# Kernel tuning notes

Measured on AMD Instinct MI355X. Metric: run time of the kernel, lower is better.

The kernel has to match this reference:

```python
import jax, jax.numpy as jnp
import numpy as np

EPS = 1e-5  # haiku LayerNorm default eps

def _ln(x):
    # LayerNorm over last dim, no scale/offset, use_fast_variance=False
    m = jnp.mean(x, axis=-1, keepdims=True)
    v = jnp.mean((x - m) ** 2, axis=-1, keepdims=True)
    return (x - m) / jnp.sqrt(v + EPS)

def _adaptive_ln(x, cond, gamma_c, Ws, bs, Wb):
    # AdaptiveLayerNorm with single_cond path
    xn = _ln(x)
    cn = _ln(cond) * gamma_c           # single_cond_layer_norm (scale only)
    scale = cn @ Ws + bs               # single_cond_scale (with bias)
    bias = cn @ Wb                     # single_cond_bias (no bias)
    return jax.nn.sigmoid(scale) * xn + bias

def setup_inputs() -> dict:
    key = jax.random.key(0)
    ks = jax.random.split(key, 24)
    B, Q, K, C, H = 2, 3072, 3072, 128, 4
    Dh = C // H
    s = 0.02
    inp = {
        'x_q': jax.random.normal(ks[0], (B, Q, C), jnp.float32),
        'x_k': jax.random.normal(ks[1], (B, K, C), jnp.float32),
        'mask_q': jax.random.randint(ks[2], (B, Q), 0, 2, jnp.int32),
        'mask_k': jax.random.randint(ks[3], (B, K), 0, 2, jnp.int32),
        'pair_logits': jax.random.normal(ks[4], (B, H, Q, K), jnp.float32),
        'single_cond_q': jax.random.normal(ks[5], (B, Q, C), jnp.float32),
        'single_cond_k': jax.random.normal(ks[6], (B, K, C), jnp.float32),
        # AdaptiveLayerNorm q params
        'gamma_cq': jnp.ones((C,), jnp.float32),
        'Wsq': jax.random.normal(ks[7], (C, C), jnp.float32) * s,
        'bsq': jax.random.normal(ks[8], (C,), jnp.float32) * s,
        'Wbq': jax.random.normal(ks[9], (C, C), jnp.float32) * s,
        # AdaptiveLayerNorm k params
        'gamma_ck': jnp.ones((C,), jnp.float32),
        'Wsk': jax.random.normal(ks[10], (C, C), jnp.float32) * s,
        'bsk': jax.random.normal(ks[11], (C,), jnp.float32) * s,
        'Wbk': jax.random.normal(ks[12], (C, C), jnp.float32) * s,
        # attention projections
        'Wq': jax.random.normal(ks[13], (C, H, Dh), jnp.float32) * s,
        'bq': jax.random.normal(ks[14], (1, H, Dh), jnp.float32) * s,
        'Wk': jax.random.normal(ks[15], (C, H, Dh), jnp.float32) * s,
        'Wv': jax.random.normal(ks[16], (C, H, Dh), jnp.float32) * s,
        'Wg': jax.random.normal(ks[17], (C, C), jnp.float32) * s,
        # AdaptiveZeroInit params
        'Wt2': jax.random.normal(ks[18], (C, C), jnp.float32) * s,
        'Wzc': jax.random.normal(ks[19], (C, C), jnp.float32) * s,
        'bzc': jax.random.normal(ks[20], (C,), jnp.float32) * s,
    }
    return inp

def reference(x_q, x_k, mask_q, mask_k, pair_logits, single_cond_q, single_cond_k,
              gamma_cq, Wsq, bsq, Wbq, gamma_ck, Wsk, bsk, Wbk,
              Wq, bq, Wk, Wv, Wg, Wt2, Wzc, bzc):
    mq = mask_q.astype(jnp.float32)
    mk = mask_k.astype(jnp.float32)
    # bias as written in the original: 1e9 * (mq-1)[...,None,:,None] * (mk-1)[...,None,None,:]
    bias = 1e9 * (mq - 1.0)[:, None, :, None] * (mk - 1.0)[:, None, None, :]
    bias = bias + pair_logits  # [B,H,Q,K]

    xq = _adaptive_ln(x_q, single_cond_q, gamma_cq, Wsq, bsq, Wbq)
    xk = _adaptive_ln(x_k, single_cond_k, gamma_ck, Wsk, bsk, Wbk)

    Dh = Wq.shape[-1]
    q = jnp.einsum('bqi,ihd->bqhd', xq, Wq) + bq  # bq [1,H,Dh] broadcasts
    k = jnp.einsum('bki,ihd->bkhd', xk, Wk)
    v = jnp.einsum('bki,ihd->bkhd', xk, Wv)

    logits = jnp.einsum('bqhd,bkhd->bhqk', q * (Dh ** -0.5), k) + bias
    weights = jax.nn.softmax(logits, axis=-1).astype(xq.dtype)
    wa = jnp.einsum('bhqk,bkhd->bqhd', weights, v)
    B, Q, H, _ = wa.shape
    wa = wa.reshape(B, Q, H * Dh)

    wa = wa * jax.nn.sigmoid(xq @ Wg)  # gating_query

    # AdaptiveZeroInit with raw single_cond_q
    out = (wa @ Wt2) * jax.nn.sigmoid(single_cond_q @ Wzc + bzc)
    return out
```

## Files before the change

kernel.cpp:

```cpp
#include <hip/hip_runtime.h>
#include <hip/hip_bf16.h>

typedef unsigned short u16;
typedef unsigned int u32;
typedef __attribute__((ext_vector_type(4))) float f32x4;
typedef __attribute__((ext_vector_type(4))) u32 u32x4;
typedef __attribute__((ext_vector_type(2))) u32 u32x2;
typedef __attribute__((ext_vector_type(8))) __bf16 bf16x8;

#define SQ 3072
#define NH 4
#define DH 32

static __device__ __forceinline__ u16 f2bf(float f) {
  return __builtin_bit_cast(u16, (__bf16)f);
}
static __device__ __forceinline__ u32 pk2(float a, float b) {
  return (u32)f2bf(a) | ((u32)f2bf(b) << 16);
}
static __device__ __forceinline__ bf16x8 ld8(const u16* p) {
  return __builtin_bit_cast(bf16x8, *reinterpret_cast<const u32x4*>(p));
}
static __device__ __forceinline__ f32x4 mfma16(bf16x8 a, bf16x8 b, f32x4 c) {
  return __builtin_amdgcn_mfma_f32_16x16x32_bf16(a, b, c, 0, 0, 0);
}
static __device__ __forceinline__ float sigm(float x) { return 1.0f / (1.0f + __expf(-x)); }
static __device__ __forceinline__ float red16(float v) {
  v += __shfl_xor(v, 1); v += __shfl_xor(v, 2);
  v += __shfl_xor(v, 4); v += __shfl_xor(v, 8);
  return v;
}

static __device__ __forceinline__ void gemm8(
    const u16* a, const u16* wt, int lr, int lg, int w, f32x4 d[2]) {
  f32x4 z = {0.f, 0.f, 0.f, 0.f};
  d[0] = z; d[1] = z;
#pragma unroll
  for (int kc = 0; kc < 4; ++kc) {
    int ko = kc * 32 + lg * 8;
    bf16x8 a0 = ld8(a + lr * 136 + ko);
    bf16x8 a1 = ld8(a + (16 + lr) * 136 + ko);
    bf16x8 b0 = ld8(wt + (w * 16 + lr) * 128 + ko);
    d[0] = mfma16(a0, b0, d[0]);
    d[1] = mfma16(a1, b0, d[1]);
  }
}

struct PrepSrc { const float* p[10]; };

__global__ __launch_bounds__(256) void prep(PrepSrc s, u16* __restrict__ dst) {
  __shared__ float tl[32][132];
  const int mm = blockIdx.x >> 2, c = blockIdx.x & 3;
  const int tid = threadIdx.x;
  {
    const int krl = tid >> 3, col0 = (tid & 7) * 16;
    const int kr = c * 32 + krl;
    const float* src = s.p[mm] + kr * 128 + col0;
#pragma unroll
    for (int j = 0; j < 4; ++j) {
      f32x4 v = *reinterpret_cast<const f32x4*>(src + j * 4);
      tl[krl][col0 + j * 4 + 0] = v[0];
      tl[krl][col0 + j * 4 + 1] = v[1];
      tl[krl][col0 + j * 4 + 2] = v[2];
      tl[krl][col0 + j * 4 + 3] = v[3];
    }
  }
  __syncthreads();
  const int co = tid >> 1, kc0 = (tid & 1) * 16;
  u32 wbuf[8];
#pragma unroll
  for (int j = 0; j < 8; ++j)
    wbuf[j] = pk2(tl[kc0 + 2 * j][co], tl[kc0 + 2 * j + 1][co]);
  u32x4* dp = reinterpret_cast<u32x4*>(dst + mm * 16384 + co * 128 + c * 32 + kc0);
  u32x4 w0 = {wbuf[0], wbuf[1], wbuf[2], wbuf[3]};
  u32x4 w1 = {wbuf[4], wbuf[5], wbuf[6], wbuf[7]};
  dp[0] = w0; dp[1] = w1;
}

__global__ __launch_bounds__(512) void rowblocks(
    const float* __restrict__ x_q, const float* __restrict__ scq,
    const float* __restrict__ gamma_cq, const float* __restrict__ bsq,
    const float* __restrict__ bq, const float* __restrict__ bzc,
    const float* __restrict__ x_k, const float* __restrict__ sck,
    const float* __restrict__ gamma_ck, const float* __restrict__ bsk,
    const u16* __restrict__ WT, const int* __restrict__ mask_k,
    u16* __restrict__ qbf, float* __restrict__ gate, float* __restrict__ zc,
    u16* __restrict__ kbf, u16* __restrict__ vT, float* __restrict__ mkf) {
  __shared__ float xnf[32 * 132];
  __shared__ u16 a_cn[32 * 136];
  __shared__ u16 a_raw[32 * 136];
  __shared__ u16 a_xa[32 * 136];
  const int tid = threadIdx.x;
  const bool qside = blockIdx.x < 192;
  const int blk = qside ? blockIdx.x : blockIdx.x - 192;
  const float* x     = qside ? x_q : x_k;
  const float* cond  = qside ? scq : sck;
  const float* gamma = qside ? gamma_cq : gamma_ck;
  const float* bs    = qside ? bsq : bsk;
  const int rl = tid >> 4, sub = tid & 15, c0 = sub * 8;
  const size_t grow = (size_t)blk * 32 + rl;
  if (!qside && tid < 32) {
    size_t g2 = (size_t)blk * 32 + tid;
    mkf[g2] = (float)mask_k[g2] - 1.f;
  }

  {
    float xs[8];
    const float4* xr = reinterpret_cast<const float4*>(x + grow * 128 + c0);
    float4 t0 = xr[0], t1 = xr[1];
    xs[0]=t0.x; xs[1]=t0.y; xs[2]=t0.z; xs[3]=t0.w;
    xs[4]=t1.x; xs[5]=t1.y; xs[6]=t1.z; xs[7]=t1.w;
    float s = 0.f;
#pragma unroll
    for (int i = 0; i < 8; ++i) s += xs[i];
    float mean = red16(s) * (1.f / 128.f);
    float vs = 0.f;
#pragma unroll
    for (int i = 0; i < 8; ++i) { float dd = xs[i] - mean; vs += dd * dd; }
    float rstd = rsqrtf(red16(vs) * (1.f / 128.f) + 1e-5f);
    float4* xw = reinterpret_cast<float4*>(&xnf[rl * 132 + c0]);
    float4 o0, o1;
    o0.x=(xs[0]-mean)*rstd; o0.y=(xs[1]-mean)*rstd; o0.z=(xs[2]-mean)*rstd; o0.w=(xs[3]-mean)*rstd;
    o1.x=(xs[4]-mean)*rstd; o1.y=(xs[5]-mean)*rstd; o1.z=(xs[6]-mean)*rstd; o1.w=(xs[7]-mean)*rstd;
    xw[0] = o0; xw[1] = o1;
  }
  {
    float cs[8], gs[8];
    const float4* cr = reinterpret_cast<const float4*>(cond + grow * 128 + c0);
    const float4* gr = reinterpret_cast<const float4*>(gamma + c0);
    float4 c_0 = cr[0], c_1 = cr[1], g_0 = gr[0], g_1 = gr[1];
    cs[0]=c_0.x; cs[1]=c_0.y; cs[2]=c_0.z; cs[3]=c_0.w;
    cs[4]=c_1.x; cs[5]=c_1.y; cs[6]=c_1.z; cs[7]=c_1.w;
    gs[0]=g_0.x; gs[1]=g_0.y; gs[2]=g_0.z; gs[3]=g_0.w;
    gs[4]=g_1.x; gs[5]=g_1.y; gs[6]=g_1.z; gs[7]=g_1.w;
    float s = 0.f;
#pragma unroll
    for (int i = 0; i < 8; ++i) s += cs[i];
    float mean = red16(s) * (1.f / 128.f);
    float vs = 0.f;
#pragma unroll
    for (int i = 0; i < 8; ++i) { float dd = cs[i] - mean; vs += dd * dd; }
    float rstd = rsqrtf(red16(vs) * (1.f / 128.f) + 1e-5f);
    float cn[8];
#pragma unroll
    for (int i = 0; i < 8; ++i) cn[i] = (cs[i] - mean) * rstd * gs[i];
    u32x4 cw = {pk2(cn[0],cn[1]), pk2(cn[2],cn[3]), pk2(cn[4],cn[5]), pk2(cn[6],cn[7])};
    *reinterpret_cast<u32x4*>(&a_cn[rl * 136 + c0]) = cw;
    if (qside) {
      u32x4 rw = {pk2(cs[0],cs[1]), pk2(cs[2],cs[3]), pk2(cs[4],cs[5]), pk2(cs[6],cs[7])};
      *reinterpret_cast<u32x4*>(&a_raw[rl * 136 + c0]) = rw;
    }
  }
  __syncthreads();
  const int lane = tid & 63, w = tid >> 6, lr = lane & 15, lg = lane >> 4;
  const int wtbase = qside ? 0 : 5;
  f32x4 dS[2], dB[2];
  gemm8(a_cn, WT + (wtbase + 0) * 16384, lr, lg, w, dS);
  gemm8(a_cn, WT + (wtbase + 1) * 16384, lr, lg, w, dB);
  const int col = w * 16 + lr;
#pragma unroll
  for (int mt = 0; mt < 2; ++mt)
#pragma unroll
    for (int r = 0; r < 4; ++r) {
      int rowl = mt * 16 + lg * 4 + r;
      float sc = dS[mt][r] + bs[col];
      float xa = sigm(sc) * xnf[rowl * 132 + col] + dB[mt][r];
      a_xa[rowl * 136 + col] = f2bf(xa);
    }
  __syncthreads();
  if (qside) {
    f32x4 dQ[2], dG[2], dZ[2];
    gemm8(a_xa,  WT + 2 * 16384, lr, lg, w, dQ);
    gemm8(a_xa,  WT + 3 * 16384, lr, lg, w, dG);
    gemm8(a_raw, WT + 4 * 16384, lr, lg, w, dZ);
#pragma unroll
    for (int mt = 0; mt < 2; ++mt)
#pragma unroll
      for (int r = 0; r < 4; ++r) {
        int rowl = mt * 16 + lg * 4 + r;
        size_t gr = (size_t)blk * 32 + rowl;
        int b = (int)(gr >= SQ);
        int pos = (int)gr - b * SQ;
        float qv = (dQ[mt][r] + bq[col]) * 0.17677669529663687f;
        qbf[(((size_t)b * NH + (col >> 5)) * SQ + pos) * DH + (col & 31)] = f2bf(qv);
        gate[gr * 128 + col] = sigm(dG[mt][r]);
        zc[gr * 128 + col] = sigm(dZ[mt][r] + bzc[col]);
      }
  } else {
    f32x4 dK[2], dV[2];
    gemm8(a_xa, WT + 7 * 16384, lr, lg, w, dK);
    gemm8(a_xa, WT + 8 * 16384, lr, lg, w, dV);
    const int h = col >> 5, dd = col & 31;
#pragma unroll
    for (int mt = 0; mt < 2; ++mt)
#pragma unroll
      for (int r = 0; r < 4; ++r) {
        int rowl = mt * 16 + lg * 4 + r;
        size_t gr = (size_t)blk * 32 + rowl;
        int b = (int)(gr >= SQ);
        int pos = (int)gr - b * SQ;
        kbf[(((size_t)b * NH + h) * SQ + pos) * DH + dd] = f2bf(dK[mt][r]);
        vT[(((size_t)b * NH + h) * DH + dd) * SQ + pos] = f2bf(dV[mt][r]);
      }
  }
}

__global__ __launch_bounds__(256) void attn(
    const u16* __restrict__ qbf, const u16* __restrict__ kbf, const u16* __restrict__ vT,
    const float* __restrict__ pair, const int* __restrict__ mask_q,
    const float* __restrict__ mkf, const float* __restrict__ gate,
    u16* __restrict__ wa) {
  __shared__ u16 pbuf[2][16][264];
  __shared__ __align__(16) char un[4][2304];
  const int tid = threadIdx.x, lane = tid & 63, w = tid >> 6, lr = lane & 15, lg = lane >> 4;
  const int bid = blockIdx.x;
  const int bh = bid & 7, qt = bid >> 3;
  const int b = bh >> 2, h = bh & 3;
  const int q0 = qt * 16;
  const bf16x8 aq = ld8(qbf + ((size_t)bh * SQ + q0 + lr) * DH + lg * 8);
  const float mqm1 = 1e9f * ((float)mask_q[b * SQ + q0 + lr] - 1.f);
  float m = -1e30f, lsum = 0.f;
  const f32x4 zero = {0.f, 0.f, 0.f, 0.f};
  f32x4 o[2]; o[0] = zero; o[1] = zero;
  const float* prow0 = pair + ((size_t)bh * SQ + q0 + w * 4) * SQ;
  const float* mrow = mkf + b * SQ;
  u16* pw = reinterpret_cast<u16*>(un[w]);
  f32x4 pf[4];
#pragma unroll
  for (int j = 0; j < 4; ++j)
    pf[j] = __builtin_nontemporal_load(
        reinterpret_cast<const f32x4*>(prow0 + (size_t)j * SQ + lane * 4));
  for (int t = 0; t < 12; ++t) {
    const int bsel = t & 1;
#pragma unroll
    for (int j = 0; j < 4; ++j) {
      u32x2 pb = {pk2(pf[j][0], pf[j][1]), pk2(pf[j][2], pf[j][3])};
      *reinterpret_cast<u32x2*>(&pbuf[bsel][w * 4 + j][lane * 4]) = pb;
    }
    __syncthreads();
    if (t < 11) {
#pragma unroll
      for (int j = 0; j < 4; ++j)
        pf[j] = __builtin_nontemporal_load(
            reinterpret_cast<const f32x4*>(prow0 + (size_t)j * SQ + (t + 1) * 256 + lane * 4));
    }
    const int kb = t * 256 + w * 64;
    f32x4 s[4];
#pragma unroll
    for (int kt = 0; kt < 4; ++kt) {
      bf16x8 kfv = ld8(kbf + ((size_t)bh * SQ + kb + kt * 16 + lr) * DH + lg * 8);
      u32x2 pd = *reinterpret_cast<const u32x2*>(&pbuf[bsel][lr][w * 64 + kt * 16 + lg * 4]);
      f32x4 pv;
      pv[0] = __builtin_bit_cast(float, (pd[0] & 0xFFFFu) << 16);
      pv[1] = __builtin_bit_cast(float, pd[0] & 0xFFFF0000u);
      pv[2] = __builtin_bit_cast(float, (pd[1] & 0xFFFFu) << 16);
      pv[3] = __builtin_bit_cast(float, pd[1] & 0xFFFF0000u);
      f32x4 mk = *reinterpret_cast<const f32x4*>(mrow + kb + kt * 16 + lg * 4);
      f32x4 c;
      c[0] = fmaf(mqm1, mk[0], pv[0]); c[1] = fmaf(mqm1, mk[1], pv[1]);
      c[2] = fmaf(mqm1, mk[2], pv[2]); c[3] = fmaf(mqm1, mk[3], pv[3]);
      s[kt] = mfma16(kfv, aq, c);
    }
    f32x4 mx = s[0];
#pragma unroll
    for (int kt = 1; kt < 4; ++kt)
#pragma unroll
      for (int r = 0; r < 4; ++r) mx[r] = fmaxf(mx[r], s[kt][r]);
    float pm = fmaxf(fmaxf(mx[0], mx[1]), fmaxf(mx[2], mx[3]));
    pm = fmaxf(pm, __shfl_xor(pm, 16));
    pm = fmaxf(pm, __shfl_xor(pm, 32));
    if (!__all(pm <= m + 8.f)) {
      const float mn = fmaxf(m, pm);
      const float alpha = __expf(m - mn);
      m = mn;
      float al[4];
#pragma unroll
      for (int r = 0; r < 4; ++r)
        al[r] = __builtin_bit_cast(
            float, __builtin_amdgcn_ds_bpermute((lg * 4 + r) << 2,
                                                __builtin_bit_cast(int, alpha)));
#pragma unroll
      for (int hf = 0; hf < 2; ++hf)
#pragma unroll
        for (int r = 0; r < 4; ++r) o[hf][r] *= al[r];
      lsum *= alpha;
    }
    float ps = 0.f;
#pragma unroll
    for (int kt = 0; kt < 4; ++kt)
#pragma unroll
      for (int r = 0; r < 4; ++r) {
        float p = __expf(s[kt][r] - m);
        s[kt][r] = p;
        ps += p;
      }
    lsum += ps;
#pragma unroll
    for (int kt = 0; kt < 4; ++kt) {
      u32x2 pk = {pk2(s[kt][0], s[kt][1]), pk2(s[kt][2], s[kt][3])};
      *reinterpret_cast<u32x2*>(pw + lr * 72 + kt * 16 + lg * 4) = pk;
    }
#pragma unroll
    for (int kc = 0; kc < 2; ++kc) {
      bf16x8 pa = ld8(pw + lr * 72 + kc * 32 + lg * 8);
#pragma unroll
      for (int hf = 0; hf < 2; ++hf) {
        bf16x8 bv = ld8(vT + ((size_t)bh * DH + hf * 16 + lr) * SQ + kb + kc * 32 + lg * 8);
        o[hf] = mfma16(pa, bv, o[hf]);
      }
    }
  }
  lsum += __shfl_xor(lsum, 16);
  lsum += __shfl_xor(lsum, 32);
  float* mbw = reinterpret_cast<float*>(un[w]);
#pragma unroll
  for (int r = 0; r < 4; ++r) {
    int row = lg * 4 + r;
    mbw[row * 34 + lr] = o[0][r];
    mbw[row * 34 + 16 + lr] = o[1][r];
  }
  if (lane < 16) { mbw[lane * 34 + 32] = m; mbw[lane * 34 + 33] = lsum; }
  __syncthreads();
#pragma unroll
  for (int it = 0; it < 2; ++it) {
    int q = (tid >> 5) + it * 8;
    int d = tid & 31;
    float mm = -1e30f;
#pragma unroll
    for (int w4 = 0; w4 < 4; ++w4)
      mm = fmaxf(mm, reinterpret_cast<const float*>(un[w4])[q * 34 + 32]);
    float ll = 0.f, oo = 0.f;
#pragma unroll
    for (int w4 = 0; w4 < 4; ++w4) {
      const float* mb4 = reinterpret_cast<const float*>(un[w4]);
      float e = __expf(mb4[q * 34 + 32] - mm);
      ll = fmaf(e, mb4[q * 34 + 33], ll);
      oo = fmaf(e, mb4[q * 34 + d], oo);
    }
    size_t gi = ((size_t)b * SQ + q0 + q) * 128 + h * 32 + d;
    wa[gi] = f2bf((oo / ll) * gate[gi]);
  }
}

__global__ __launch_bounds__(512) void finalk(
    const u16* __restrict__ wa, const u16* __restrict__ WTt2,
    const float* __restrict__ zc, float* __restrict__ out) {
  __shared__ u16 awa[32 * 136];
  const int tid = threadIdx.x, rl = tid >> 4, sub = tid & 15, c0 = sub * 8;
  const size_t grow = (size_t)blockIdx.x * 32 + rl;
  *reinterpret_cast<u32x4*>(&awa[rl * 136 + c0]) =
      *reinterpret_cast<const u32x4*>(wa + grow * 128 + c0);
  __syncthreads();
  const int lane = tid & 63, w = tid >> 6, lr = lane & 15, lg = lane >> 4;
  f32x4 d[2];
  gemm8(awa, WTt2, lr, lg, w, d);
  const int col = w * 16 + lr;
#pragma unroll
  for (int mt = 0; mt < 2; ++mt)
#pragma unroll
    for (int r = 0; r < 4; ++r) {
      size_t gr = (size_t)blockIdx.x * 32 + mt * 16 + lg * 4 + r;
      out[gr * 128 + col] = d[mt][r] * zc[gr * 128 + col];
    }
}

extern "C" void kernel_launch(void* const* d_in, const int* in_sizes, int n_in,
                              void* d_out, int out_size, void* d_ws, size_t ws_size,
                              hipStream_t stream) {
  const float* x_q   = (const float*)d_in[0];
  const float* x_k   = (const float*)d_in[1];
  const int* mask_q  = (const int*)d_in[2];
  const int* mask_k  = (const int*)d_in[3];
  const float* pair  = (const float*)d_in[4];
  const float* scq   = (const float*)d_in[5];
  const float* sck   = (const float*)d_in[6];
  const float* gamma_cq = (const float*)d_in[7];
  const float* Wsq   = (const float*)d_in[8];
  const float* bsq   = (const float*)d_in[9];
  const float* Wbq   = (const float*)d_in[10];
  const float* gamma_ck = (const float*)d_in[11];
  const float* Wsk   = (const float*)d_in[12];
  const float* bsk   = (const float*)d_in[13];
  const float* Wbk   = (const float*)d_in[14];
  const float* Wq    = (const float*)d_in[15];
  const float* bq    = (const float*)d_in[16];
  const float* Wk    = (const float*)d_in[17];
  const float* Wv    = (const float*)d_in[18];
  const float* Wg    = (const float*)d_in[19];
  const float* Wt2   = (const float*)d_in[20];
  const float* Wzc   = (const float*)d_in[21];
  const float* bzc   = (const float*)d_in[22];

  char* wsb = (char*)d_ws;
  u16* WT     = (u16*)(wsb);
  u16* qbf    = (u16*)(wsb + 327680);
  u16* kbf    = (u16*)(wsb + 1900544);
  u16* vT     = (u16*)(wsb + 3473408);
  float* gate = (float*)(wsb + 5046272);
  float* zc   = (float*)(wsb + 8192000);
  u16* wa     = (u16*)(wsb + 11337728);
  float* mkf  = (float*)(wsb + 12910592);
  float* out  = (float*)d_out;

  PrepSrc ps;
  ps.p[0] = Wsq; ps.p[1] = Wbq; ps.p[2] = Wq; ps.p[3] = Wg; ps.p[4] = Wzc;
  ps.p[5] = Wsk; ps.p[6] = Wbk; ps.p[7] = Wk; ps.p[8] = Wv; ps.p[9] = Wt2;

  hipLaunchKernelGGL(prep, dim3(40), dim3(256), 0, stream, ps, WT);
  hipLaunchKernelGGL(rowblocks, dim3(384), dim3(512), 0, stream,
                     x_q, scq, gamma_cq, bsq, bq, bzc,
                     x_k, sck, gamma_ck, bsk, WT, mask_k,
                     qbf, gate, zc, kbf, vT, mkf);
  hipLaunchKernelGGL(attn, dim3(8 * 192), dim3(256), 0, stream,
                     qbf, kbf, vT, pair, mask_q, mkf, gate, wa);
  hipLaunchKernelGGL(finalk, dim3(192), dim3(512), 0, stream, wa, WT + 9 * 16384, zc, out);
}
```

Before: 117.4 us.

## Deepen pair-logit prefetch pipeline to triple-buffered LDS with two register sets

The attention kernel's streaming of pair logits moves from a double-buffered LDS with one register prefetch stage to a triple-buffered LDS fed by two alternating register sets. Global loads are issued up to four tiles ahead, and the loop is fully unrolled. The aim is to hide HBM latency on the dominant pair_logits read, which is about 300MB of fp32. The cost is more VGPRs and more LDS per block, which may lower occupancy.

```diff
diff --git a/kernel.cpp b/kernel.cpp
--- a/kernel.cpp
+++ b/kernel.cpp
@@ -210,7 +210,7 @@
     const float* __restrict__ pair, const int* __restrict__ mask_q,
     const float* __restrict__ mkf, const float* __restrict__ gate,
     u16* __restrict__ wa) {
-  __shared__ u16 pbuf[2][16][264];
+  __shared__ u16 pbuf[3][16][264];
   __shared__ __align__(16) char un[4][2304];
   const int tid = threadIdx.x, lane = tid & 63, w = tid >> 6, lr = lane & 15, lg = lane >> 4;
   const int bid = blockIdx.x;
@@ -225,31 +225,37 @@
   const float* prow0 = pair + ((size_t)bh * SQ + q0 + w * 4) * SQ;
   const float* mrow = mkf + b * SQ;
   u16* pw = reinterpret_cast<u16*>(un[w]);
-  f32x4 pf[4];
-#pragma unroll
-  for (int j = 0; j < 4; ++j)
-    pf[j] = __builtin_nontemporal_load(
-        reinterpret_cast<const f32x4*>(prow0 + (size_t)j * SQ + lane * 4));
+
+  f32x4 pA[4], pB[4];
+#define ISSUE(g, R)                                                              \
+  {                                                                              \
+    _Pragma("unroll") for (int j = 0; j < 4; ++j) R[j] =                         \
+        __builtin_nontemporal_load(reinterpret_cast<const f32x4*>(               \
+            prow0 + (size_t)j * SQ + (g) * 256 + lane * 4));                     \
+  }
+#define STORE(g, R)                                                              \
+  {                                                                              \
+    _Pragma("unroll") for (int j = 0; j < 4; ++j) {                              \
+      u32x2 pb = {pk2(R[j][0], R[j][1]), pk2(R[j][2], R[j][3])};                 \
+      *reinterpret_cast<u32x2*>(&pbuf[(g) % 3][w * 4 + j][lane * 4]) = pb;       \
+    }                                                                            \
+  }
+  ISSUE(0, pA); ISSUE(1, pB);
+  STORE(0, pA); ISSUE(2, pA);
+  STORE(1, pB); ISSUE(3, pB);
+#pragma unroll
   for (int t = 0; t < 12; ++t) {
-    const int bsel = t & 1;
-#pragma unroll
-    for (int j = 0; j < 4; ++j) {
-      u32x2 pb = {pk2(pf[j][0], pf[j][1]), pk2(pf[j][2], pf[j][3])};
-      *reinterpret_cast<u32x2*>(&pbuf[bsel][w * 4 + j][lane * 4]) = pb;
-    }
     __syncthreads();
-    if (t < 11) {
-#pragma unroll
-      for (int j = 0; j < 4; ++j)
-        pf[j] = __builtin_nontemporal_load(
-            reinterpret_cast<const f32x4*>(prow0 + (size_t)j * SQ + (t + 1) * 256 + lane * 4));
+    if (t + 2 < 12) {
+      if ((t & 1) == 0) { STORE(t + 2, pA); if (t + 4 < 12) ISSUE(t + 4, pA); }
+      else              { STORE(t + 2, pB); if (t + 4 < 12) ISSUE(t + 4, pB); }
     }
     const int kb = t * 256 + w * 64;
     f32x4 s[4];
 #pragma unroll
     for (int kt = 0; kt < 4; ++kt) {
       bf16x8 kfv = ld8(kbf + ((size_t)bh * SQ + kb + kt * 16 + lr) * DH + lg * 8);
-      u32x2 pd = *reinterpret_cast<const u32x2*>(&pbuf[bsel][lr][w * 64 + kt * 16 + lg * 4]);
+      u32x2 pd = *reinterpret_cast<const u32x2*>(&pbuf[t % 3][lr][w * 64 + kt * 16 + lg * 4]);
       f32x4 pv;
       pv[0] = __builtin_bit_cast(float, (pd[0] & 0xFFFFu) << 16);
       pv[1] = __builtin_bit_cast(float, pd[0] & 0xFFFF0000u);
@@ -310,6 +316,8 @@
       }
     }
   }
+#undef ISSUE
+#undef STORE
   lsum += __shfl_xor(lsum, 16);
   lsum += __shfl_xor(lsum, 32);
   float* mbw = reinterpret_cast<float*>(un[w]);
```

Result: no change. 118.9 us (+1.3%).

## Process 32 query rows per attention block to reuse K, V and mask loads

Applied to the files above, without the earlier changes.

Each attention workgroup now handles two 16-row query groups instead of one, so every K tile, V tile and key-mask vector loaded from global memory feeds two MFMA groups. The grid halves to 768 blocks, and each thread prefetches twice as many pair_logits rows. The pair_logits loads also switch from nontemporal to normal loads. The cost is higher register and LDS use per block, which may lower occupancy, and fewer blocks to spread across the CUs.

```diff
diff --git a/kernel.cpp b/kernel.cpp
--- a/kernel.cpp
+++ b/kernel.cpp
@@ -210,119 +210,154 @@
     const float* __restrict__ pair, const int* __restrict__ mask_q,
     const float* __restrict__ mkf, const float* __restrict__ gate,
     u16* __restrict__ wa) {
-  __shared__ u16 pbuf[2][16][264];
-  __shared__ __align__(16) char un[4][2304];
+  __shared__ u16 pbuf[2][32][264];
+  __shared__ __align__(16) char un[4][4608];
   const int tid = threadIdx.x, lane = tid & 63, w = tid >> 6, lr = lane & 15, lg = lane >> 4;
   const int bid = blockIdx.x;
   const int bh = bid & 7, qt = bid >> 3;
   const int b = bh >> 2, h = bh & 3;
-  const int q0 = qt * 16;
-  const bf16x8 aq = ld8(qbf + ((size_t)bh * SQ + q0 + lr) * DH + lg * 8);
-  const float mqm1 = 1e9f * ((float)mask_q[b * SQ + q0 + lr] - 1.f);
-  float m = -1e30f, lsum = 0.f;
+  const int q0 = qt * 32;
+  bf16x8 aq[2];
+  float mqm1[2];
+#pragma unroll
+  for (int qg = 0; qg < 2; ++qg) {
+    aq[qg] = ld8(qbf + ((size_t)bh * SQ + q0 + qg * 16 + lr) * DH + lg * 8);
+    mqm1[qg] = 1e9f * ((float)mask_q[b * SQ + q0 + qg * 16 + lr] - 1.f);
+  }
+  float m[2] = {-1e30f, -1e30f}, lsum[2] = {0.f, 0.f};
   const f32x4 zero = {0.f, 0.f, 0.f, 0.f};
-  f32x4 o[2]; o[0] = zero; o[1] = zero;
-  const float* prow0 = pair + ((size_t)bh * SQ + q0 + w * 4) * SQ;
+  f32x4 o[2][2];
+  o[0][0] = zero; o[0][1] = zero; o[1][0] = zero; o[1][1] = zero;
+  const float* prow0 = pair + ((size_t)bh * SQ + q0 + w * 8) * SQ;
   const float* mrow = mkf + b * SQ;
   u16* pw = reinterpret_cast<u16*>(un[w]);
-  f32x4 pf[4];
-#pragma unroll
-  for (int j = 0; j < 4; ++j)
-    pf[j] = __builtin_nontemporal_load(
-        reinterpret_cast<const f32x4*>(prow0 + (size_t)j * SQ + lane * 4));
+  f32x4 pf[8];
+#pragma unroll
+  for (int j = 0; j < 8; ++j)
+    pf[j] = *reinterpret_cast<const f32x4*>(prow0 + (size_t)j * SQ + lane * 4);
   for (int t = 0; t < 12; ++t) {
     const int bsel = t & 1;
 #pragma unroll
-    for (int j = 0; j < 4; ++j) {
+    for (int j = 0; j < 8; ++j) {
       u32x2 pb = {pk2(pf[j][0], pf[j][1]), pk2(pf[j][2], pf[j][3])};
-      *reinterpret_cast<u32x2*>(&pbuf[bsel][w * 4 + j][lane * 4]) = pb;
+      *reinterpret_cast<u32x2*>(&pbuf[bsel][w * 8 + j][lane * 4]) = pb;
     }
     __syncthreads();
     if (t < 11) {
 #pragma unroll
-      for (int j = 0; j < 4; ++j)
-        pf[j] = __builtin_nontemporal_load(
-            reinterpret_cast<const f32x4*>(prow0 + (size_t)j * SQ + (t + 1) * 256 + lane * 4));
+      for (int j = 0; j < 8; ++j)
+        pf[j] = *reinterpret_cast<const f32x4*>(prow0 + (size_t)j * SQ + (t + 1) * 256 + lane * 4);
     }
     const int kb = t * 256 + w * 64;
-    f32x4 s[4];
+    bf16x8 kf[4];
+    f32x4 mk[4];
 #pragma unroll
     for (int kt = 0; kt < 4; ++kt) {
-      bf16x8 kfv = ld8(kbf + ((size_t)bh * SQ + kb + kt * 16 + lr) * DH + lg * 8);
-      u32x2 pd = *reinterpret_cast<const u32x2*>(&pbuf[bsel][lr][w * 64 + kt * 16 + lg * 4]);
-      f32x4 pv;
-      pv[0] = __builtin_bit_cast(float, (pd[0] & 0xFFFFu) << 16);
-      pv[1] = __builtin_bit_cast(float, pd[0] & 0xFFFF0000u);
-      pv[2] = __builtin_bit_cast(float, (pd[1] & 0xFFFFu) << 16);
-      pv[3] = __builtin_bit_cast(float, pd[1] & 0xFFFF0000u);
-      f32x4 mk = *reinterpret_cast<const f32x4*>(mrow + kb + kt * 16 + lg * 4);
-      f32x4 c;
-      c[0] = fmaf(mqm1, mk[0], pv[0]); c[1] = fmaf(mqm1, mk[1], pv[1]);
-      c[2] = fmaf(mqm1, mk[2], pv[2]); c[3] = fmaf(mqm1, mk[3], pv[3]);
-      s[kt] = mfma16(kfv, aq, c);
-    }
-    f32x4 mx = s[0];
-#pragma unroll
-    for (int kt = 1; kt < 4; ++kt)
-#pragma unroll
-      for (int r = 0; r < 4; ++r) mx[r] = fmaxf(mx[r], s[kt][r]);
-    float pm = fmaxf(fmaxf(mx[0], mx[1]), fmaxf(mx[2], mx[3]));
-    pm = fmaxf(pm, __shfl_xor(pm, 16));
-    pm = fmaxf(pm, __shfl_xor(pm, 32));
-    if (!__all(pm <= m + 8.f)) {
-      const float mn = fmaxf(m, pm);
-      const float alpha = __expf(m - mn);
-      m = mn;
-      float al[4];
-#pragma unroll
-      for (int r = 0; r < 4; ++r)
-        al[r] = __builtin_bit_cast(
-            float, __builtin_amdgcn_ds_bpermute((lg * 4 + r) << 2,
-                                                __builtin_bit_cast(int, alpha)));
-#pragma unroll
-      for (int hf = 0; hf < 2; ++hf)
-#pragma unroll
-        for (int r = 0; r < 4; ++r) o[hf][r] *= al[r];
-      lsum *= alpha;
-    }
-    float ps = 0.f;
-#pragma unroll
-    for (int kt = 0; kt < 4; ++kt)
-#pragma unroll
-      for (int r = 0; r < 4; ++r) {
-        float p = __expf(s[kt][r] - m);
-        s[kt][r] = p;
-        ps += p;
-      }
-    lsum += ps;
-#pragma unroll
-    for (int kt = 0; kt < 4; ++kt) {
-      u32x2 pk = {pk2(s[kt][0], s[kt][1]), pk2(s[kt][2], s[kt][3])};
-      *reinterpret_cast<u32x2*>(pw + lr * 72 + kt * 16 + lg * 4) = pk;
-    }
-#pragma unroll
-    for (int kc = 0; kc < 2; ++kc) {
-      bf16x8 pa = ld8(pw + lr * 72 + kc * 32 + lg * 8);
+      kf[kt] = ld8(kbf + ((size_t)bh * SQ + kb + kt * 16 + lr) * DH + lg * 8);
+      mk[kt] = *reinterpret_cast<const f32x4*>(mrow + kb + kt * 16 + lg * 4);
+    }
+    f32x4 s[2][4];
+#pragma unroll
+    for (int qg = 0; qg < 2; ++qg)
+#pragma unroll
+      for (int kt = 0; kt < 4; ++kt) {
+        u32x2 pd = *reinterpret_cast<const u32x2*>(
+            &pbuf[bsel][qg * 16 + lr][w * 64 + kt * 16 + lg * 4]);
+        f32x4 pv;
+        pv[0] = __builtin_bit_cast(float, (pd[0] & 0xFFFFu) << 16);
+        pv[1] = __builtin_bit_cast(float, pd[0] & 0xFFFF0000u);
+        pv[2] = __builtin_bit_cast(float, (pd[1] & 0xFFFFu) << 16);
+        pv[3] = __builtin_bit_cast(float, pd[1] & 0xFFFF0000u);
+        f32x4 c;
+        c[0] = fmaf(mqm1[qg], mk[kt][0], pv[0]);
+        c[1] = fmaf(mqm1[qg], mk[kt][1], pv[1]);
+        c[2] = fmaf(mqm1[qg], mk[kt][2], pv[2]);
+        c[3] = fmaf(mqm1[qg], mk[kt][3], pv[3]);
+        s[qg][kt] = mfma16(kf[kt], aq[qg], c);
+      }
+    float pm[2];
+#pragma unroll
+    for (int qg = 0; qg < 2; ++qg) {
+      f32x4 mx = s[qg][0];
+#pragma unroll
+      for (int kt = 1; kt < 4; ++kt)
+#pragma unroll
+        for (int r = 0; r < 4; ++r) mx[r] = fmaxf(mx[r], s[qg][kt][r]);
+      float p = fmaxf(fmaxf(mx[0], mx[1]), fmaxf(mx[2], mx[3]));
+      p = fmaxf(p, __shfl_xor(p, 16));
+      p = fmaxf(p, __shfl_xor(p, 32));
+      pm[qg] = p;
+    }
+    if (!__all((pm[0] <= m[0] + 8.f) && (pm[1] <= m[1] + 8.f))) {
+#pragma unroll
+      for (int qg = 0; qg < 2; ++qg) {
+        const float mn = fmaxf(m[qg], pm[qg]);
+        const float alpha = __expf(m[qg] - mn);
+        m[qg] = mn;
+        float al[4];
+#pragma unroll
+        for (int r = 0; r < 4; ++r)
+          al[r] = __builtin_bit_cast(
+              float, __builtin_amdgcn_ds_bpermute((lg * 4 + r) << 2,
+                                                  __builtin_bit_cast(int, alpha)));
+#pragma unroll
+        for (int hf = 0; hf < 2; ++hf)
+#pragma unroll
+          for (int r = 0; r < 4; ++r) o[qg][hf][r] *= al[r];
+        lsum[qg] *= alpha;
+      }
+    }
+#pragma unroll
+    for (int qg = 0; qg < 2; ++qg) {
+      float ps = 0.f;
+#pragma unroll
+      for (int kt = 0; kt < 4; ++kt) {
+#pragma unroll
+        for (int r = 0; r < 4; ++r) {
+          float p = __expf(s[qg][kt][r] - m[qg]);
+          s[qg][kt][r] = p;
+          ps += p;
+        }
+        u32x2 pk = {pk2(s[qg][kt][0], s[qg][kt][1]), pk2(s[qg][kt][2], s[qg][kt][3])};
+        *reinterpret_cast<u32x2*>(pw + (qg * 16 + lr) * 72 + kt * 16 + lg * 4) = pk;
+      }
+      lsum[qg] += ps;
+    }
+#pragma unroll
+    for (int kc = 0; kc < 2; ++kc)
 #pragma unroll
       for (int hf = 0; hf < 2; ++hf) {
         bf16x8 bv = ld8(vT + ((size_t)bh * DH + hf * 16 + lr) * SQ + kb + kc * 32 + lg * 8);
-        o[hf] = mfma16(pa, bv, o[hf]);
-      }
-    }
-  }
-  lsum += __shfl_xor(lsum, 16);
-  lsum += __shfl_xor(lsum, 32);
+#pragma unroll
+        for (int qg = 0; qg < 2; ++qg) {
+          bf16x8 pa = ld8(pw + (qg * 16 + lr) * 72 + kc * 32 + lg * 8);
+          o[qg][hf] = mfma16(pa, bv, o[qg][hf]);
+        }
+      }
+  }
+#pragma unroll
+  for (int qg = 0; qg < 2; ++qg) {
+    lsum[qg] += __shfl_xor(lsum[qg], 16);
+    lsum[qg] += __shfl_xor(lsum[qg], 32);
+  }
+  __syncthreads();
   float* mbw = reinterpret_cast<float*>(un[w]);
 #pragma unroll
-  for (int r = 0; r < 4; ++r) {
-    int row = lg * 4 + r;
-    mbw[row * 34 + lr] = o[0][r];
-    mbw[row * 34 + 16 + lr] = o[1][r];
-  }
-  if (lane < 16) { mbw[lane * 34 + 32] = m; mbw[lane * 34 + 33] = lsum; }
-  __syncthreads();
-#pragma unroll
-  for (int it = 0; it < 2; ++it) {
+  for (int qg = 0; qg < 2; ++qg) {
+#pragma unroll
+    for (int r = 0; r < 4; ++r) {
+      int row = qg * 16 + lg * 4 + r;
+      mbw[row * 34 + lr] = o[qg][0][r];
+      mbw[row * 34 + 16 + lr] = o[qg][1][r];
+    }
+    if (lane < 16) {
+      mbw[(qg * 16 + lane) * 34 + 32] = m[qg];
+      mbw[(qg * 16 + lane) * 34 + 33] = lsum[qg];
+    }
+  }
+  __syncthreads();
+#pragma unroll
+  for (int it = 0; it < 4; ++it) {
     int q = (tid >> 5) + it * 8;
     int d = tid & 31;
     float mm = -1e30f;
@@ -411,7 +446,7 @@
                      x_q, scq, gamma_cq, bsq, bq, bzc,
                      x_k, sck, gamma_ck, bsk, WT, mask_k,
                      qbf, gate, zc, kbf, vT, mkf);
-  hipLaunchKernelGGL(attn, dim3(8 * 192), dim3(256), 0, stream,
+  hipLaunchKernelGGL(attn, dim3(8 * 96), dim3(256), 0, stream,
                      qbf, kbf, vT, pair, mask_q, mkf, gate, wa);
   hipLaunchKernelGGL(finalk, dim3(192), dim3(512), 0, stream, wa, WT + 9 * 16384, zc, out);
 }
```

Result: faster. 112.9 us (median of 2 runs) (-3.8%).
